# Performance work log

Measured on AMD Instinct MI355X. Metric: run time of the kernel, lower is better.

The kernel has to match this reference:

```python
import jax, jax.numpy as jnp
import numpy as np

N, K, D = 131072, 64, 256


def setup_inputs() -> dict:
    key = jax.random.key(0)
    k1, k2, k3, k4, k5 = jax.random.split(key, 5)
    X = jax.random.normal(k1, (N, D), dtype=jnp.float32)
    # mixture weights: positive, sum to 1 (log is taken)
    weights = jax.nn.softmax(jax.random.normal(k2, (K,), dtype=jnp.float32))
    means = jax.random.normal(k3, (K, D), dtype=jnp.float32)
    # precision Cholesky factors: lower-triangular with positive diagonal
    tril = jnp.tril(0.01 * jax.random.normal(k4, (K, D, D), dtype=jnp.float32), k=-1)
    diag = 0.5 + jax.random.uniform(k5, (K, D), dtype=jnp.float32)  # in (0.5, 1.5)
    precision_cholesky = tril + jax.vmap(jnp.diag)(diag)
    return {"X": X, "weights": weights, "means": means,
            "precision_cholesky": precision_cholesky}


def reference(X, weights, means, precision_cholesky):
    n_samples, n_features = X.shape
    # log|L_k| = sum of log of diagonal entries (sklearn's strided-diagonal trick)
    log_det = jnp.sum(jnp.log(jnp.diagonal(precision_cholesky, axis1=1, axis2=2)), axis=1)  # (K,)

    # Per-component Mahalanobis distance, sequential over K to avoid an [N,K,D] buffer
    def mahalanobis(args):
        mu, prec_chol = args                      # (D,), (D,D)
        y = X @ prec_chol - mu @ prec_chol        # (N,D)
        return jnp.sum(y * y, axis=1)             # (N,)

    sq = jax.lax.map(mahalanobis, (means, precision_cholesky))  # (K,N)

    log_prob = -0.5 * (n_features * jnp.log(2.0 * jnp.pi) + sq.T) + log_det  # (N,K)
    weighted_log_prob = log_prob + jnp.log(weights)                          # (N,K)
    log_prob_norm = jax.nn.logsumexp(weighted_log_prob, axis=1)              # (N,)
    log_resp = weighted_log_prob - log_prob_norm[:, None]                    # (N,K)
    return jnp.mean(log_prob_norm), log_resp
```

## Files before the change

kernel.cpp:

```cpp
#include <hip/hip_runtime.h>
#include <hip/hip_bf16.h>
#include <cmath>


typedef unsigned short ushort_t;
typedef __attribute__((ext_vector_type(4))) float f32x4;
typedef __attribute__((ext_vector_type(8))) short bf16x8;

constexpr int N_ = 131072;
constexpr int K_ = 64;
constexpr int D_ = 256;
constexpr int BM = 128;
constexpr int NBLK = N_ / BM;

__device__ __forceinline__ ushort_t f2bf(float v) {
  unsigned u = __float_as_uint(v);
  u += 0x7FFFu + ((u >> 16) & 1u);
  return (ushort_t)(u >> 16);
}

__device__ __forceinline__ void gld16(const ushort_t* g, ushort_t* l) {
  __builtin_amdgcn_global_load_lds(
      (const __attribute__((address_space(1))) unsigned int*)g,
      (__attribute__((address_space(3))) unsigned int*)l, 16, 0, 0);
}

__device__ __forceinline__ float dpp_red16(float v) {
  int x = __float_as_int(v);
  v += __int_as_float(__builtin_amdgcn_update_dpp(0, x, 0xB1, 0xF, 0xF, true));
  x = __float_as_int(v);
  v += __int_as_float(__builtin_amdgcn_update_dpp(0, x, 0x4E, 0xF, 0xF, true));
  x = __float_as_int(v);
  v += __int_as_float(__builtin_amdgcn_update_dpp(0, x, 0x141, 0xF, 0xF, true));
  x = __float_as_int(v);
  v += __int_as_float(__builtin_amdgcn_update_dpp(0, x, 0x140, 0xF, 0xF, true));
  return v;
}

__global__ void prep_x(const float* __restrict__ X, ushort_t* __restrict__ Xb) {
  for (int e = blockIdx.x * blockDim.x + threadIdx.x; e < N_ * D_;
       e += gridDim.x * blockDim.x) {
    int j = e & 7;
    int lane = (e >> 3) & 63;
    int kc = (e >> 9) & 7;
    int mm = (e >> 12) & 7;
    int T = e >> 15;
    int row = T * 128 + mm * 16 + (lane & 15);
    int col = kc * 32 + (lane >> 4) * 8 + j;
    Xb[e] = f2bf(X[(size_t)row * D_ + col]);
  }
}

__global__ void prep_p(const float* __restrict__ P, ushort_t* __restrict__ Pb) {
  for (int e = blockIdx.x * blockDim.x + threadIdx.x; e < K_ * D_ * D_;
       e += gridDim.x * blockDim.x) {
    int j = e & 7;
    int lane = (e >> 3) & 63;
    int n = (e >> 9) & 3;
    int wc = (e >> 11) & 3;
    int g = e >> 13;
    int k = g >> 3, s = g & 7;
    int row_p = s * 32 + (lane >> 4) * 8 + j;
    int col_p = wc * 64 + n * 16 + (lane & 15);
    Pb[e] = f2bf(P[((size_t)k * D_ + row_p) * D_ + col_p]);
  }
}

__global__ void prep_t(const float* __restrict__ P, const float* __restrict__ mu,
                       const float* __restrict__ w, ushort_t* __restrict__ Ub,
                       float* __restrict__ C2) {
  int k = blockIdx.x, j = threadIdx.x;
  const float* Pk = P + (size_t)k * D_ * D_;
  const float* muk = mu + (size_t)k * D_;
  __shared__ float tl[D_];
  __shared__ float red[D_];
  float acc = 0.f;
  for (int i = 0; i < D_; ++i) acc += muk[i] * Pk[(size_t)i * D_ + j];
  tl[j] = acc;
  red[j] = acc * acc;
  __syncthreads();
  for (int s = 128; s > 0; s >>= 1) {
    if (j < s) red[j] += red[j + s];
    __syncthreads();
  }
  float tn = red[0];
  __syncthreads();
  red[j] = logf(Pk[(size_t)j * D_ + j]);
  __syncthreads();
  for (int s = 128; s > 0; s >>= 1) {
    if (j < s) red[j] += red[j + s];
    __syncthreads();
  }
  if (j == 0)
    C2[k] = red[0] + logf(w[k]) - 0.5f * (float)D_ * logf(2.0f * (float)M_PI) -
            0.5f * tn;
  float u = 0.f;
  for (int jj = 0; jj < D_; ++jj) u += Pk[(size_t)j * D_ + jj] * tl[jj];
  int e = ((j >> 5) * 4 + (k >> 4)) * 512 +
          (((j >> 3) & 3) * 16 + (k & 15)) * 8 + (j & 7);
  Ub[e] = f2bf(u);
}

__global__ __launch_bounds__(512, 2) void gmm_main(
    const ushort_t* __restrict__ Xb, const ushort_t* __restrict__ Pb,
    const ushort_t* __restrict__ Ub,
    float* __restrict__ wlp ) {
  __shared__ __align__(16) ushort_t Bl[8 * 8192];
  __shared__ float sqf[BM * K_];

  const int tid = threadIdx.x;
  const int T = blockIdx.x;
  const int lane = tid & 63, wid = tid >> 6;
  const int wr = wid >> 2, wc = wid & 3;
  const int lc = lane & 15, lg = lane >> 4;

#pragma unroll
  for (int i = 0; i < 16; ++i) sqf[tid + i * 512] = 0.f;

  const ushort_t* Ag = Xb + (size_t)T * 32768;
  bf16x8 Areg[32];
#pragma unroll
  for (int m = 0; m < 4; ++m)
#pragma unroll
    for (int c = 0; c < 8; ++c)
      Areg[m * 8 + c] =
          *(const bf16x8*)&Ag[(((wr * 4 + m) * 8 + c) * 512) + lane * 8];

#pragma unroll
  for (int g0 = 0; g0 < 4; ++g0)
#pragma unroll
    for (int it = 0; it < 2; ++it)
      gld16(Pb + (size_t)g0 * 8192 + (it * 512 + tid) * 8,
            &Bl[g0 * 8192 + (it * 512 + tid) * 8]);
  asm volatile("s_waitcnt vmcnt(0) lgkmcnt(0)" ::: "memory");
  __builtin_amdgcn_s_barrier();

#pragma unroll 1
  for (int k = 0; k < K_; ++k) {
    f32x4 acc[4][4];
#pragma unroll
    for (int m = 0; m < 4; ++m)
#pragma unroll
      for (int n = 0; n < 4; ++n) acc[m][n] = (f32x4){0.f, 0.f, 0.f, 0.f};

#pragma unroll
    for (int s = 0; s < 8; s += 2) {
      int g4 = k * 8 + s + 4;
      if (g4 > 511) g4 = 511;
      int g5 = k * 8 + s + 5;
      if (g5 > 511) g5 = 511;
      {
        const ushort_t* p4 = Pb + (size_t)g4 * 8192;
        ushort_t* d4 = &Bl[((s + 4) & 7) * 8192];
#pragma unroll
        for (int it = 0; it < 2; ++it)
          gld16(p4 + (it * 512 + tid) * 8, d4 + (it * 512 + tid) * 8);
      }
      {
        const ushort_t* p5 = Pb + (size_t)g5 * 8192;
        ushort_t* d5 = &Bl[((s + 5) & 7) * 8192];
#pragma unroll
        for (int it = 0; it < 2; ++it)
          gld16(p5 + (it * 512 + tid) * 8, d5 + (it * 512 + tid) * 8);
      }
      asm volatile("s_waitcnt vmcnt(8)" ::: "memory");
      __builtin_amdgcn_s_barrier();

#pragma unroll
      for (int h = 0; h < 2; ++h) {
        const int ss = s + h;
        bf16x8 bb[4];
#pragma unroll
        for (int n = 0; n < 4; ++n)
          bb[n] =
              *(const bf16x8*)&Bl[ss * 8192 + (wc * 4 + n) * 512 + lane * 8];
#pragma unroll
        for (int m = 0; m < 4; ++m)
#pragma unroll
          for (int n = 0; n < 4; ++n)
            acc[m][n] = __builtin_amdgcn_mfma_f32_16x16x32_bf16(
                Areg[m * 8 + ss], bb[n], acc[m][n], 0, 0, 0);
      }
    }

#pragma unroll
    for (int m = 0; m < 4; ++m)
#pragma unroll
      for (int r = 0; r < 4; ++r) {
        float a0 = acc[m][0][r], a1 = acc[m][1][r];
        float a2 = acc[m][2][r], a3 = acc[m][3][r];
        float sfl = dpp_red16(a0 * a0 + a1 * a1 + a2 * a2 + a3 * a3);
        if (lc == 0) {
          int row = wr * 64 + m * 16 + lg * 4 + r;
          atomicAdd(&sqf[row * 64 + k], sfl);
        }
      }
  }

  bf16x8 Uf[8];
#pragma unroll
  for (int c = 0; c < 8; ++c)
    Uf[c] = *(const bf16x8*)&Ub[(c * 4 + wc) * 512 + lane * 8];
  f32x4 accd[4];
#pragma unroll
  for (int m = 0; m < 4; ++m) accd[m] = (f32x4){0.f, 0.f, 0.f, 0.f};
#pragma unroll
  for (int c = 0; c < 8; ++c)
#pragma unroll
    for (int m = 0; m < 4; ++m)
      accd[m] = __builtin_amdgcn_mfma_f32_16x16x32_bf16(Areg[m * 8 + c], Uf[c],
                                                        accd[m], 0, 0, 0);
#pragma unroll
  for (int m = 0; m < 4; ++m)
#pragma unroll
    for (int r = 0; r < 4; ++r) {
      int row = wr * 64 + m * 16 + lg * 4 + r;
      atomicAdd(&sqf[row * 64 + wc * 16 + lc], -2.0f * accd[m][r]);
    }

  __syncthreads();

  float* dst = wlp + (size_t)T * BM * K_;
#pragma unroll
  for (int i = 0; i < 4; ++i) {
    int idx4 = tid + i * 512;
    ((f32x4*)dst)[idx4] = *(const f32x4*)&sqf[idx4 * 4];
  }
}

__global__ void lse_k(float* __restrict__ out, const float* __restrict__ C2,
                      float* __restrict__ partial) {
  __shared__ float C2l[K_];
  if (threadIdx.x < K_) C2l[threadIdx.x] = C2[threadIdx.x];
  __syncthreads();
  const int row = blockIdx.x * 256 + threadIdx.x;
  float* w = out + 1 + (size_t)row * K_;
  float v[K_];
  float mx = -1e30f;
#pragma unroll
  for (int j = 0; j < K_; ++j) {
    v[j] = -0.5f * w[j] + C2l[j];
    mx = fmaxf(mx, v[j]);
  }
  float ssum = 0.f;
#pragma unroll
  for (int j = 0; j < K_; ++j) ssum += expf(v[j] - mx);
  float l = mx + logf(ssum);
#pragma unroll
  for (int j = 0; j < K_; ++j) w[j] = v[j] - l;
  __shared__ float red[256];
  red[threadIdx.x] = l;
  __syncthreads();
  for (int s = 128; s > 0; s >>= 1) {
    if (threadIdx.x < s) red[threadIdx.x] += red[threadIdx.x + s];
    __syncthreads();
  }
  if (threadIdx.x == 0) partial[blockIdx.x] = red[0];
}

__global__ void final_red(const float* __restrict__ partial,
                          float* __restrict__ out) {
  __shared__ float red[512];
  red[threadIdx.x] = partial[threadIdx.x];
  __syncthreads();
  for (int s = 256; s > 0; s >>= 1) {
    if (threadIdx.x < s) red[threadIdx.x] += red[threadIdx.x + s];
    __syncthreads();
  }
  if (threadIdx.x == 0) out[0] = red[0] * (1.0f / (float)N_);
}

extern "C" void kernel_launch(void* const* d_in, const int* in_sizes, int n_in,
                              void* d_out, int out_size, void* d_ws,
                              size_t ws_size, hipStream_t stream) {
  const float* X = (const float*)d_in[0];
  const float* w = (const float*)d_in[1];
  const float* mu = (const float*)d_in[2];
  const float* P = (const float*)d_in[3];
  float* out = (float*)d_out;
  char* ws = (char*)d_ws;

  ushort_t* Xb = (ushort_t*)ws;
  ushort_t* Pb = (ushort_t*)(ws + 67108864);
  ushort_t* Ub = (ushort_t*)(ws + 75497472);
  float* C2 = (float*)(ws + 75530240);
  float* partial = (float*)(ws + 75530496);

  prep_x<<<2048, 256, 0, stream>>>(X, Xb);
  prep_p<<<2048, 256, 0, stream>>>(P, Pb);
  prep_t<<<K_, 256, 0, stream>>>(P, mu, w, Ub, C2);
  gmm_main<<<NBLK, 512, 0, stream>>>(Xb, Pb, Ub, out + 1);
  lse_k<<<N_ / 256, 256, 0, stream>>>(out, C2, partial);
  final_red<<<1, 512, 0, stream>>>(partial, out);
}
```

Before: 1.006 ms.

## Split mixture components across eight blocks per row tile

```diff
diff --git a/kernel.cpp b/kernel.cpp
--- a/kernel.cpp
+++ b/kernel.cpp
@@ -11,7 +11,7 @@
 constexpr int K_ = 64;
 constexpr int D_ = 256;
 constexpr int BM = 128;
-constexpr int NBLK = N_ / BM;
+constexpr int NBLK = (N_ / BM) * 8;
 
 __device__ __forceinline__ ushort_t f2bf(float v) {
   unsigned u = __float_as_uint(v);
@@ -96,8 +96,8 @@
             0.5f * tn;
   float u = 0.f;
   for (int jj = 0; jj < D_; ++jj) u += Pk[(size_t)j * D_ + jj] * tl[jj];
-  int e = ((j >> 5) * 4 + (k >> 4)) * 512 +
-          (((j >> 3) & 3) * 16 + (k & 15)) * 8 + (j & 7);
+  int lane = (k & 7) + 16 * ((j >> 3) & 3);
+  int e = ((k >> 3) * 8 + (j >> 5)) * 512 + lane * 8 + (j & 7);
   Ub[e] = f2bf(u);
 }
 
@@ -106,16 +106,20 @@
     const ushort_t* __restrict__ Ub,
     float* __restrict__ wlp ) {
   __shared__ __align__(16) ushort_t Bl[8 * 8192];
-  __shared__ float sqf[BM * K_];
+  __shared__ float sqf[BM * 8];
 
   const int tid = threadIdx.x;
-  const int T = blockIdx.x;
+  const int bid = blockIdx.x;
+  const int T = bid >> 3;
+  const int rng = bid & 7;
+  const int k0 = rng * 8;
+
   const int lane = tid & 63, wid = tid >> 6;
   const int wr = wid >> 2, wc = wid & 3;
   const int lc = lane & 15, lg = lane >> 4;
 
-#pragma unroll
-  for (int i = 0; i < 16; ++i) sqf[tid + i * 512] = 0.f;
+  sqf[tid] = 0.f;
+  sqf[tid + 512] = 0.f;
 
   const ushort_t* Ag = Xb + (size_t)T * 32768;
   bf16x8 Areg[32];
@@ -126,17 +130,18 @@
       Areg[m * 8 + c] =
           *(const bf16x8*)&Ag[(((wr * 4 + m) * 8 + c) * 512) + lane * 8];
 
+  const ushort_t* Pbase = Pb + (size_t)k0 * 65536;
 #pragma unroll
   for (int g0 = 0; g0 < 4; ++g0)
 #pragma unroll
     for (int it = 0; it < 2; ++it)
-      gld16(Pb + (size_t)g0 * 8192 + (it * 512 + tid) * 8,
+      gld16(Pbase + (size_t)g0 * 8192 + (it * 512 + tid) * 8,
             &Bl[g0 * 8192 + (it * 512 + tid) * 8]);
   asm volatile("s_waitcnt vmcnt(0) lgkmcnt(0)" ::: "memory");
   __builtin_amdgcn_s_barrier();
 
 #pragma unroll 1
-  for (int k = 0; k < K_; ++k) {
+  for (int kk = 0; kk < 8; ++kk) {
     f32x4 acc[4][4];
 #pragma unroll
     for (int m = 0; m < 4; ++m)
@@ -144,20 +149,21 @@
       for (int n = 0; n < 4; ++n) acc[m][n] = (f32x4){0.f, 0.f, 0.f, 0.f};
 
 #pragma unroll
-    for (int s = 0; s < 8; s += 2) {
-      int g4 = k * 8 + s + 4;
-      if (g4 > 511) g4 = 511;
-      int g5 = k * 8 + s + 5;
-      if (g5 > 511) g5 = 511;
+    for (int w = 0; w < 4; ++w) {
+      const int s = 2 * w;
+      int L4 = kk * 8 + s + 4;
+      if (L4 > 63) L4 = 63;
+      int L5 = kk * 8 + s + 5;
+      if (L5 > 63) L5 = 63;
       {
-        const ushort_t* p4 = Pb + (size_t)g4 * 8192;
+        const ushort_t* p4 = Pbase + (size_t)L4 * 8192;
         ushort_t* d4 = &Bl[((s + 4) & 7) * 8192];
 #pragma unroll
         for (int it = 0; it < 2; ++it)
           gld16(p4 + (it * 512 + tid) * 8, d4 + (it * 512 + tid) * 8);
       }
       {
-        const ushort_t* p5 = Pb + (size_t)g5 * 8192;
+        const ushort_t* p5 = Pbase + (size_t)L5 * 8192;
         ushort_t* d5 = &Bl[((s + 5) & 7) * 8192];
 #pragma unroll
         for (int it = 0; it < 2; ++it)
@@ -192,39 +198,41 @@
         float sfl = dpp_red16(a0 * a0 + a1 * a1 + a2 * a2 + a3 * a3);
         if (lc == 0) {
           int row = wr * 64 + m * 16 + lg * 4 + r;
-          atomicAdd(&sqf[row * 64 + k], sfl);
+          atomicAdd(&sqf[row * 8 + kk], sfl);
         }
       }
   }
 
-  bf16x8 Uf[8];
-#pragma unroll
-  for (int c = 0; c < 8; ++c)
-    Uf[c] = *(const bf16x8*)&Ub[(c * 4 + wc) * 512 + lane * 8];
+  bf16x8 Uf[2];
+#pragma unroll
+  for (int c2 = 0; c2 < 2; ++c2)
+    Uf[c2] = *(const bf16x8*)&Ub[((size_t)rng * 8 + wc * 2 + c2) * 512 +
+                                 lane * 8];
   f32x4 accd[4];
 #pragma unroll
   for (int m = 0; m < 4; ++m) accd[m] = (f32x4){0.f, 0.f, 0.f, 0.f};
 #pragma unroll
-  for (int c = 0; c < 8; ++c)
+  for (int c2 = 0; c2 < 2; ++c2)
 #pragma unroll
     for (int m = 0; m < 4; ++m)
-      accd[m] = __builtin_amdgcn_mfma_f32_16x16x32_bf16(Areg[m * 8 + c], Uf[c],
-                                                        accd[m], 0, 0, 0);
+      accd[m] = __builtin_amdgcn_mfma_f32_16x16x32_bf16(
+          Areg[m * 8 + wc * 2 + c2], Uf[c2], accd[m], 0, 0, 0);
 #pragma unroll
   for (int m = 0; m < 4; ++m)
 #pragma unroll
     for (int r = 0; r < 4; ++r) {
-      int row = wr * 64 + m * 16 + lg * 4 + r;
-      atomicAdd(&sqf[row * 64 + wc * 16 + lc], -2.0f * accd[m][r]);
+      if (lc < 8) {
+        int row = wr * 64 + m * 16 + lg * 4 + r;
+        atomicAdd(&sqf[row * 8 + lc], -2.0f * accd[m][r]);
+      }
     }
 
   __syncthreads();
 
-  float* dst = wlp + (size_t)T * BM * K_;
-#pragma unroll
-  for (int i = 0; i < 4; ++i) {
-    int idx4 = tid + i * 512;
-    ((f32x4*)dst)[idx4] = *(const f32x4*)&sqf[idx4 * 4];
+  if (tid < 256) {
+    int row = tid >> 1, half = tid & 1;
+    float* dst = wlp + ((size_t)(T * 128 + row)) * 64 + k0 + half * 4;
+    *(f32x4*)dst = *(const f32x4*)&sqf[row * 8 + half * 4];
   }
 }
 
@@ -283,9 +291,10 @@
   ushort_t* Xb = (ushort_t*)ws;
   ushort_t* Pb = (ushort_t*)(ws + 67108864);
   ushort_t* Ub = (ushort_t*)(ws + 75497472);
-  float* C2 = (float*)(ws + 75530240);
-  float* partial = (float*)(ws + 75530496);
-
+  float* C2 = (float*)(ws + 75563008);
+  float* partial = (float*)(ws + 75563264);
+
+  hipMemsetAsync(Ub, 0, 65536, stream);
   prep_x<<<2048, 256, 0, stream>>>(X, Xb);
   prep_p<<<2048, 256, 0, stream>>>(P, Pb);
   prep_t<<<K_, 256, 0, stream>>>(P, mu, w, Ub, C2);
```

New measurement: 1.788 ms. +77.7%, slower.
